# Kernel optimization log

Measured on AMD Instinct MI355X. Metric: run time of the kernel, lower is better.

Reference implementation:

```python
import jax, jax.numpy as jnp
import numpy as np

B, V, D = 8, 2048, 3
CL1_F, CL1_K = 64, 6
CL2_F, CL2_K = 128, 5
F1, F2 = 512, 256


def _uniform(k, shape, fin, fout):
    s = np.sqrt(2.0 / (fin + fout)).astype(np.float32)
    return jax.random.uniform(k, shape, jnp.float32, -s, s)


def setup_inputs() -> dict:
    key = jax.random.key(0)
    ks = jax.random.split(key, 8)
    x = jax.random.normal(ks[0], (B, D, V), jnp.float32)
    # dense stand-in for the scaled graph Laplacian; scaled so spectral radius < 1
    L = jax.random.normal(ks[1], (B, V, V), jnp.float32) * (0.5 / np.sqrt(V))
    L = 0.5 * (L + L.transpose(0, 2, 1))  # symmetric like a real Laplacian
    return {
        "x": x,
        "L": L,
        "cl1_w": _uniform(ks[2], (CL1_F, D * CL1_K), CL1_K, CL1_F),
        "cl1_b": jnp.zeros((CL1_F,), jnp.float32),
        "cl2_w": _uniform(ks[3], (CL2_F, CL2_K * CL1_F), CL2_K * CL1_F, CL2_F),
        "cl2_b": jnp.zeros((CL2_F,), jnp.float32),
        "fc1_w": _uniform(ks[4], (F1, CL2_F), CL2_F, F1),
        "fc1_b": jnp.zeros((F1,), jnp.float32),
        "fc2_w": _uniform(ks[5], (F2, F1), F1, F2),
        "fc2_b": jnp.zeros((F2,), jnp.float32),
    }


def _cheby_conv(x, L, W, b, K):
    # x: [B, V, Fin], L: [B, V, V] -> [B, V, Fout]
    x0 = x
    xs = [x0]
    if K > 1:
        x1 = jnp.einsum('bvu,buf->bvf', L, x0)
        xs.append(x1)
    for _ in range(2, K):
        x2 = 2.0 * jnp.einsum('bvu,buf->bvf', L, x1) - x0
        xs.append(x2)
        x0, x1 = x1, x2
    # torch ordering: feature index = fin * K + k  -> stack K on last axis
    xk = jnp.stack(xs, axis=-1)                 # [B, V, Fin, K]
    xk = xk.reshape(xk.shape[0], xk.shape[1], -1)  # [B, V, Fin*K]
    return xk @ W.T + b


def reference(x, L, cl1_w, cl1_b, cl2_w, cl2_b, fc1_w, fc1_b, fc2_w, fc2_b):
    xp = x.transpose(0, 2, 1)                    # [B, V, D]
    y = jax.nn.relu(_cheby_conv(xp, L, cl1_w, cl1_b, CL1_K))
    y = jax.nn.relu(_cheby_conv(y, L, cl2_w, cl2_b, CL2_K))
    y = jax.nn.relu(y @ fc1_w.T + fc1_b)
    y = jax.nn.relu(y @ fc2_w.T + fc2_b)
    return y                                     # [B, V, F2]
```

## Files before the change

kernel.cpp:

```cpp
#include <hip/hip_runtime.h>

#define B_ 8
#define V_ 2048
#define D_ 3
#define M_ (B_*V_)

typedef __attribute__((ext_vector_type(8))) short short8;
typedef __attribute__((ext_vector_type(4))) float f32x4;

__device__ inline void async_copy16(const void* g, void* lds) {
  __builtin_amdgcn_global_load_lds(
      (const __attribute__((address_space(1))) unsigned int*)g,
      (__attribute__((address_space(3))) unsigned int*)lds, 16, 0, 0);
}

__device__ inline void split_bf16(float v, short& hi, short& lo) {
  unsigned u  = __float_as_uint(v);
  unsigned hb = u & 0xFFFF0000u;
  float d = v - __uint_as_float(hb);
  hi = (short)(hb >> 16);
  lo = (short)(__float_as_uint(d) >> 16);
}

__global__ __launch_bounds__(256) void k_prep(
    const float* __restrict__ x,
    const float* __restrict__ w1, const float* __restrict__ w2,
    const float* __restrict__ fw1, const float* __restrict__ fw2,
    float* __restrict__ xa,
    short* __restrict__ XKh, short* __restrict__ XKl,
    short* __restrict__ w1h, short* __restrict__ w1l,
    short* __restrict__ w2h, short* __restrict__ w2l,
    short* __restrict__ fw1h, short* __restrict__ fw1l,
    short* __restrict__ fw2h, short* __restrict__ fw2l) {
  int i = blockIdx.x * 256 + threadIdx.x;
  short hi, lo;
  if (i < M_*64) {
    int r = i >> 6, s = i & 63;
    float val = 0.f;
    if (s == 0 || s == 6 || s == 12) {
      int f = s / 6;
      int b = r >> 11, v = r & (V_-1);
      val = x[((size_t)b*D_ + f)*V_ + v];
      xa[(size_t)r*3 + f] = val;
    }
    split_bf16(val, hi, lo);
    XKh[i] = hi; XKl[i] = lo;
    return;
  }
  i -= M_*64;
  if (i < 4096) {
    int n = i >> 6, k = i & 63;
    float v = (k < 18) ? w1[n*18 + k] : 0.f;
    split_bf16(v, hi, lo); w1h[i] = hi; w1l[i] = lo; return;
  }
  i -= 4096;
  if (i < 40960) { split_bf16(w2[i],  hi, lo); w2h[i]=hi;  w2l[i]=lo;  return; }
  i -= 40960;
  if (i < 65536) { split_bf16(fw1[i], hi, lo); fw1h[i]=hi; fw1l[i]=lo; return; }
  i -= 65536;
  if (i < 131072){ split_bf16(fw2[i], hi, lo); fw2h[i]=hi; fw2l[i]=lo; return; }
}

__global__ __launch_bounds__(256) void k_cheby1(const float* __restrict__ L,
    const float* __restrict__ xc, const float* __restrict__ xp,
    float* __restrict__ xn, short* __restrict__ XKh, short* __restrict__ XKl,
    float alpha, float beta, int kidx) {
  __shared__ float sx[3][V_];
  int b  = blockIdx.x & 7;
  int r0 = (blockIdx.x >> 3) * 16;
  const float* xcb = xc + (size_t)b*V_*D_;
  for (int i = threadIdx.x; i < V_*D_; i += 256) {
    int u = i / 3, f = i - u*3;
    sx[f][u] = xcb[i];
  }
  __syncthreads();
  int w = threadIdx.x >> 6, lane = threadIdx.x & 63;
  const float4* X0 = (const float4*)sx[0];
  const float4* X1 = (const float4*)sx[1];
  const float4* X2 = (const float4*)sx[2];
  int rbase = r0 + w*4;
  const float4* Lr[4];
  #pragma unroll
  for (int rr = 0; rr < 4; rr++)
    Lr[rr] = (const float4*)(L + ((size_t)b*V_ + rbase + rr)*V_);

  float acc[4][3] = {{0.f,0.f,0.f},{0.f,0.f,0.f},{0.f,0.f,0.f},{0.f,0.f,0.f}};

  #pragma unroll 2
  for (int it = 0; it < 8; it++) {
    int u4 = it*64 + lane;
    float4 x0 = X0[u4], x1 = X1[u4], x2 = X2[u4];
    #pragma unroll
    for (int rr = 0; rr < 4; rr++) {
      float4 lv = Lr[rr][u4];
      acc[rr][0] = fmaf(lv.x,x0.x,fmaf(lv.y,x0.y,fmaf(lv.z,x0.z,fmaf(lv.w,x0.w,acc[rr][0]))));
      acc[rr][1] = fmaf(lv.x,x1.x,fmaf(lv.y,x1.y,fmaf(lv.z,x1.z,fmaf(lv.w,x1.w,acc[rr][1]))));
      acc[rr][2] = fmaf(lv.x,x2.x,fmaf(lv.y,x2.y,fmaf(lv.z,x2.z,fmaf(lv.w,x2.w,acc[rr][2]))));
    }
  }
  #pragma unroll
  for (int off = 32; off > 0; off >>= 1)
    #pragma unroll
    for (int rr = 0; rr < 4; rr++)
      #pragma unroll
      for (int f = 0; f < 3; f++)
        acc[rr][f] += __shfl_down(acc[rr][f], off);

  if (lane == 0) {
    size_t base = ((size_t)b*V_ + rbase)*3;
    float v[12];
    #pragma unroll
    for (int rr = 0; rr < 4; rr++)
      #pragma unroll
      for (int f = 0; f < 3; f++)
        v[rr*3+f] = alpha*acc[rr][f];
    if (beta != 0.f) {
      const float4* xp4 = (const float4*)(xp + base);
      float4 p0 = xp4[0], p1 = xp4[1], p2 = xp4[2];
      v[0] -= beta*p0.x; v[1]  -= beta*p0.y; v[2]  -= beta*p0.z; v[3]  -= beta*p0.w;
      v[4] -= beta*p1.x; v[5]  -= beta*p1.y; v[6]  -= beta*p1.z; v[7]  -= beta*p1.w;
      v[8] -= beta*p2.x; v[9]  -= beta*p2.y; v[10] -= beta*p2.z; v[11] -= beta*p2.w;
    }
    float4* xn4 = (float4*)(xn + base);
    xn4[0] = make_float4(v[0], v[1], v[2],  v[3]);
    xn4[1] = make_float4(v[4], v[5], v[6],  v[7]);
    xn4[2] = make_float4(v[8], v[9], v[10], v[11]);
    #pragma unroll
    for (int rr = 0; rr < 4; rr++)
      #pragma unroll
      for (int f = 0; f < 3; f++) {
        short hi, lo; split_bf16(v[rr*3+f], hi, lo);
        size_t o = ((size_t)b*V_ + rbase + rr)*64 + f*6 + kidx;
        XKh[o] = hi; XKl[o] = lo;
      }
  }
}

__global__ __launch_bounds__(256) void k_cheby2_mfma(const float* __restrict__ L,
    const short* __restrict__ Zth, const short* __restrict__ Ztl,
    const float* __restrict__ Zp,
    float* __restrict__ Zn, short* __restrict__ ZKh, short* __restrict__ ZKl,
    short* __restrict__ Znth, short* __restrict__ Zntl,
    float alpha, float beta, int kidx) {
  __shared__ float sA[2][32*64];
  __shared__ short sBh[2][64*64];
  __shared__ short sBl[2][64*64];

  int b  = blockIdx.x & 7;
  int r0 = (blockIdx.x >> 3) * 32;
  const float* Lb   = L   + (size_t)b*V_*V_;
  const short* Zthb = Zth + (size_t)b*64*V_;
  const short* Ztlb = Ztl + (size_t)b*64*V_;

  int tid  = threadIdx.x;
  int w    = tid >> 6;
  int lane = tid & 63;
  int lm   = lane & 15;
  int quad = lane >> 4;
  int cbase = w * 16;

  int f1  = tid + 256;
  int rA0 = tid >> 4, cA0 = (tid & 15) ^ (rA0 & 15);
  int rA1 = f1 >> 4,  cA1 = (f1 & 15) ^ (rA1 & 15);
  size_t gA0 = (size_t)(r0 + rA0)*V_ + cA0*4;
  size_t gA1 = (size_t)(r0 + rA1)*V_ + cA1*4;
  int nB0 = tid >> 3, cB0 = (tid & 7) ^ (nB0 & 7);
  int nB1 = f1 >> 3,  cB1 = (f1 & 7) ^ (nB1 & 7);
  size_t gB0 = (size_t)nB0*V_ + cB0*8;
  size_t gB1 = (size_t)nB1*V_ + cB1*8;

  auto stage = [&](int bb, int k0) {
    async_copy16(Lb   + gA0 + k0, &sA[bb][tid*4]);
    async_copy16(Lb   + gA1 + k0, &sA[bb][f1*4]);
    async_copy16(Zthb + gB0 + k0, &sBh[bb][tid*8]);
    async_copy16(Ztlb + gB0 + k0, &sBl[bb][tid*8]);
    async_copy16(Zthb + gB1 + k0, &sBh[bb][f1*8]);
    async_copy16(Ztlb + gB1 + k0, &sBl[bb][f1*8]);
  };

  f32x4 acc[2] = {{0.f,0.f,0.f,0.f},{0.f,0.f,0.f,0.f}};

  stage(0, 0);

  for (int s = 0; s < V_/64; s++) {
    int bb = s & 1;
    asm volatile("s_waitcnt vmcnt(0)" ::: "memory");
    __builtin_amdgcn_s_barrier();
    __builtin_amdgcn_sched_barrier(0);
    if (s < V_/64 - 1) stage(bb ^ 1, (s+1)*64);

    const f32x4*  sAv  = (const f32x4*)sA[bb];
    const short8* sBhv = (const short8*)sBh[bb];
    const short8* sBlv = (const short8*)sBl[bb];

    #pragma unroll
    for (int ks = 0; ks < 2; ks++) {
      int koff = ks * 32;
      short8 ah[2], al[2];
      #pragma unroll
      for (int t = 0; t < 2; t++) {
        int r = t*16 + lm;
        int ca = (koff >> 2) + 2*quad;
        f32x4 a0 = sAv[r*16 + (ca ^ (r & 15))];
        f32x4 a1 = sAv[r*16 + ((ca + 1) ^ (r & 15))];
        float av[8] = {a0.x, a0.y, a0.z, a0.w, a1.x, a1.y, a1.z, a1.w};
        #pragma unroll
        for (int j = 0; j < 8; j++) {
          short hi, lo; split_bf16(av[j], hi, lo);
          ah[t][j] = hi; al[t][j] = lo;
        }
      }
      int cb = (koff >> 3) + quad;
      int n = cbase + lm;
      short8 bh = sBhv[n*8 + (cb ^ (n & 7))];
      short8 bl = sBlv[n*8 + (cb ^ (n & 7))];
      __builtin_amdgcn_s_setprio(1);
      #pragma unroll
      for (int t = 0; t < 2; t++) {
        acc[t] = __builtin_amdgcn_mfma_f32_16x16x32_bf16(ah[t], bh, acc[t], 0, 0, 0);
        acc[t] = __builtin_amdgcn_mfma_f32_16x16x32_bf16(ah[t], bl, acc[t], 0, 0, 0);
        acc[t] = __builtin_amdgcn_mfma_f32_16x16x32_bf16(al[t], bh, acc[t], 0, 0, 0);
      }
      __builtin_amdgcn_s_setprio(0);
    }
  }

  int n = cbase + lm;
  #pragma unroll
  for (int t = 0; t < 2; t++) {
    #pragma unroll
    for (int i = 0; i < 4; i++) {
      int r = r0 + t*16 + quad*4 + i;
      size_t rowb = (size_t)b*V_ + r;
      float v = alpha * acc[t][i];
      if (beta != 0.f) v -= beta * Zp[rowb*64 + n];
      Zn[rowb*64 + n] = v;
      short hi, lo; split_bf16(v, hi, lo);
      size_t ok = rowb*320 + (size_t)n*5 + kidx;
      ZKh[ok] = hi; ZKl[ok] = lo;
      size_t o = ((size_t)b*64 + n)*V_ + r;
      Znth[o] = hi; Zntl[o] = lo;
    }
  }
}

__device__ __forceinline__ void gemm_tile(
    const short* __restrict__ Ah, const short* __restrict__ Al,
    const short* __restrict__ Wh, const short* __restrict__ Wl,
    const float* __restrict__ bias, int N, int K, int row0, int col0,
    short* sAh, short* sAl, short* sWh, short* sWl,
    float* __restrict__ Cf, short* __restrict__ Ch, short* __restrict__ Cl,
    short* __restrict__ Ph, short* __restrict__ Pl, int packMul, int packStride,
    short* __restrict__ Th, short* __restrict__ Tl) {
  int tid = threadIdx.x, w = tid >> 6, lane = tid & 63;
  int lm = lane & 15, quad = lane >> 4;
  int wm = (w & 1) * 32, wn = (w >> 1) * 32;

  const short8* vAh = (const short8*)sAh;
  const short8* vAl = (const short8*)sAl;
  const short8* vWh = (const short8*)sWh;
  const short8* vWl = (const short8*)sWl;

  f32x4 acc[2][2] = {{{0.f,0.f,0.f,0.f},{0.f,0.f,0.f,0.f}},
                     {{0.f,0.f,0.f,0.f},{0.f,0.f,0.f,0.f}}};

  for (int k0 = 0; k0 < K; k0 += 64) {
    if (k0) __syncthreads();
    #pragma unroll
    for (int t = 0; t < 2; t++) {
      int f = t*256 + tid;
      int r = f >> 3, p = f & 7;
      int c = p ^ (r & 7);
      size_t goA = (size_t)(row0 + r)*K + k0 + c*8;
      size_t goW = (size_t)(col0 + r)*K + k0 + c*8;
      async_copy16(Ah + goA, &sAh[f*8]);
      async_copy16(Al + goA, &sAl[f*8]);
      async_copy16(Wh + goW, &sWh[f*8]);
      async_copy16(Wl + goW, &sWl[f*8]);
    }
    __syncthreads();

    #pragma unroll
    for (int ks = 0; ks < 2; ks++) {
      int kc = ks*4 + quad;
      short8 a_h[2], a_l[2], b_h[2], b_l[2];
      #pragma unroll
      for (int i = 0; i < 2; i++) {
        int m = wm + i*16 + lm;
        a_h[i] = vAh[m*8 + (kc ^ (m & 7))];
        a_l[i] = vAl[m*8 + (kc ^ (m & 7))];
      }
      #pragma unroll
      for (int j = 0; j < 2; j++) {
        int n = wn + j*16 + lm;
        b_h[j] = vWh[n*8 + (kc ^ (n & 7))];
        b_l[j] = vWl[n*8 + (kc ^ (n & 7))];
      }
      #pragma unroll
      for (int i = 0; i < 2; i++)
        #pragma unroll
        for (int j = 0; j < 2; j++) {
          acc[i][j] = __builtin_amdgcn_mfma_f32_16x16x32_bf16(a_h[i], b_h[j], acc[i][j], 0, 0, 0);
          acc[i][j] = __builtin_amdgcn_mfma_f32_16x16x32_bf16(a_h[i], b_l[j], acc[i][j], 0, 0, 0);
          acc[i][j] = __builtin_amdgcn_mfma_f32_16x16x32_bf16(a_l[i], b_h[j], acc[i][j], 0, 0, 0);
        }
    }
  }

  #pragma unroll
  for (int i = 0; i < 2; i++)
    #pragma unroll
    for (int j = 0; j < 2; j++) {
      int col = col0 + wn + j*16 + lm;
      float bj = bias[col];
      #pragma unroll
      for (int g = 0; g < 4; g++) {
        int row = row0 + wm + i*16 + quad*4 + g;
        float v = acc[i][j][g] + bj;
        v = v > 0.f ? v : 0.f;
        if (Cf) Cf[(size_t)row*N + col] = v;
        short hi, lo;
        if (Ch || Ph || Th) split_bf16(v, hi, lo);
        if (Ch) {
          Ch[(size_t)row*N + col] = hi;
          Cl[(size_t)row*N + col] = lo;
        }
        if (Ph) {
          size_t o = (size_t)row*packStride + (size_t)col*packMul;
          Ph[o] = hi; Pl[o] = lo;
        }
        if (Th) {
          int bb = row >> 11, vv = row & (V_-1);
          size_t o = ((size_t)bb*64 + col)*V_ + vv;
          Th[o] = hi; Tl[o] = lo;
        }
      }
    }
}

__global__ __launch_bounds__(256) void k_gemm_y1(
    const short* __restrict__ XKh, const short* __restrict__ XKl,
    const short* __restrict__ w1h, const short* __restrict__ w1l,
    const float* __restrict__ b1, float* __restrict__ y1,
    short* __restrict__ ZKh, short* __restrict__ ZKl,
    short* __restrict__ Th, short* __restrict__ Tl) {
  __shared__ short sAh[64*64], sAl[64*64], sWh[64*64], sWl[64*64];
  gemm_tile(XKh, XKl, w1h, w1l, b1, 64, 64, blockIdx.x*64, 0,
            sAh, sAl, sWh, sWl,
            y1, nullptr, nullptr, ZKh, ZKl, 5, 320, Th, Tl);
}

__global__ __launch_bounds__(256) void k_gemm_bf16(
    const short* __restrict__ Ah, const short* __restrict__ Al,
    const short* __restrict__ Wh, const short* __restrict__ Wl,
    const float* __restrict__ bias, int N, int K,
    float* __restrict__ Cf, short* __restrict__ Ch, short* __restrict__ Cl) {
  __shared__ short sAh[64*64], sAl[64*64], sWh[64*64], sWl[64*64];
  int bm = blockIdx.x & 255;
  int bn = blockIdx.x >> 8;
  gemm_tile(Ah, Al, Wh, Wl, bias, N, K, bm*64, bn*64,
            sAh, sAl, sWh, sWl,
            Cf, Ch, Cl, nullptr, nullptr, 0, 0, nullptr, nullptr);
}

extern "C" void kernel_launch(void* const* d_in, const int* in_sizes, int n_in,
                              void* d_out, int out_size, void* d_ws, size_t ws_size,
                              hipStream_t stream) {
  const float* x   = (const float*)d_in[0];
  const float* L   = (const float*)d_in[1];
  const float* w1  = (const float*)d_in[2];
  const float* b1  = (const float*)d_in[3];
  const float* w2  = (const float*)d_in[4];
  const float* b2  = (const float*)d_in[5];
  const float* fw1 = (const float*)d_in[6];
  const float* fb1 = (const float*)d_in[7];
  const float* fw2 = (const float*)d_in[8];
  const float* fb2 = (const float*)d_in[9];
  float* out = (float*)d_out;

  float* p  = (float*)d_ws;
  float* xa = p;  p += (size_t)B_*V_*D_;
  float* xb = p;  p += (size_t)B_*V_*D_;
  float* xc = p;  p += (size_t)B_*V_*D_;
  float* y1 = p;  p += (size_t)M_*64;
  float* zb = p;  p += (size_t)M_*64;
  float* zc = p;  p += (size_t)M_*64;
  short* sp = (short*)p;
  short* ZKh = sp;  sp += (size_t)M_*320;
  short* ZKl = sp;  sp += (size_t)M_*320;
  short* y2h = sp;  sp += (size_t)M_*128;
  short* y2l = sp;  sp += (size_t)M_*128;
  short* h1h = sp;  sp += (size_t)M_*512;
  short* h1l = sp;  sp += (size_t)M_*512;
  short* ZtAh = sp; sp += (size_t)M_*64;
  short* ZtAl = sp; sp += (size_t)M_*64;
  short* ZtBh = sp; sp += (size_t)M_*64;
  short* ZtBl = sp; sp += (size_t)M_*64;
  short* w1h = sp;  sp += 64*64;
  short* w1l = sp;  sp += 64*64;
  short* w2h = sp;  sp += 128*320;
  short* w2l = sp;  sp += 128*320;
  short* fw1h = sp; sp += 512*128;
  short* fw1l = sp; sp += 512*128;
  short* fw2h = sp; sp += 256*512;
  short* fw2l = sp; sp += 256*512;
  short* XKh = h1h;
  short* XKl = h1h + (size_t)M_*64;

  k_prep<<<5040, 256, 0, stream>>>(x, w1, w2, fw1, fw2, xa,
                                   XKh, XKl, w1h, w1l, w2h, w2l,
                                   fw1h, fw1l, fw2h, fw2l);

  k_cheby1<<<1024, 256, 0, stream>>>(L, xa, xa, xb, XKh, XKl, 1.f, 0.f, 1);
  k_cheby1<<<1024, 256, 0, stream>>>(L, xb, xa, xc, XKh, XKl, 2.f, 1.f, 2);
  k_cheby1<<<1024, 256, 0, stream>>>(L, xc, xb, xa, XKh, XKl, 2.f, 1.f, 3);
  k_cheby1<<<1024, 256, 0, stream>>>(L, xa, xc, xb, XKh, XKl, 2.f, 1.f, 4);
  k_cheby1<<<1024, 256, 0, stream>>>(L, xb, xa, xc, XKh, XKl, 2.f, 1.f, 5);

  k_gemm_y1<<<256, 256, 0, stream>>>(XKh, XKl, w1h, w1l, b1,
                                     y1, ZKh, ZKl, ZtAh, ZtAl);

  k_cheby2_mfma<<<512, 256, 0, stream>>>(L, ZtAh, ZtAl, y1, zb, ZKh, ZKl,
                                         ZtBh, ZtBl, 1.f, 0.f, 1);
  k_cheby2_mfma<<<512, 256, 0, stream>>>(L, ZtBh, ZtBl, y1, zc, ZKh, ZKl,
                                         ZtAh, ZtAl, 2.f, 1.f, 2);
  k_cheby2_mfma<<<512, 256, 0, stream>>>(L, ZtAh, ZtAl, zb, y1, ZKh, ZKl,
                                         ZtBh, ZtBl, 2.f, 1.f, 3);
  k_cheby2_mfma<<<512, 256, 0, stream>>>(L, ZtBh, ZtBl, zc, zb, ZKh, ZKl,
                                         ZtAh, ZtAl, 2.f, 1.f, 4);

  k_gemm_bf16<<<512, 256, 0, stream>>>(ZKh, ZKl, w2h, w2l, b2, 128, 320,
                                       nullptr, y2h, y2l);
  k_gemm_bf16<<<2048, 256, 0, stream>>>(y2h, y2l, fw1h, fw1l, fb1, 512, 128,
                                        nullptr, h1h, h1l);
  k_gemm_bf16<<<1024, 256, 0, stream>>>(h1h, h1l, fw2h, fw2l, fb2, 256, 512,
                                        out, nullptr, nullptr);
}
```

Measured before the change: 536.4 us.

## Fuse all stages into one persistent kernel with software grid barriers

Replaces the sequence of separate kernel launches with one persistent kernel of 512 blocks. The blocks step through every phase (prep, five Chebyshev-1 steps, the first GEMM, four Chebyshev-2 MFMA steps, three GEMMs) and wait at an atomic-counter grid barrier between phases. The aim is to drop per-launch overhead and the tail idle time at each kernel boundary. The cheby1 phase now processes 32 rows per block, and the GEMM phases loop over multiple tiles per block. The kernel depends on all 512 blocks being resident at once (launch_bounds 256,2) to avoid deadlock, and the shared-memory union plus fixed grid size may limit occupancy.

```diff
diff --git a/kernel.cpp b/kernel.cpp
--- a/kernel.cpp
+++ b/kernel.cpp
@@ -4,6 +4,7 @@
 #define V_ 2048
 #define D_ 3
 #define M_ (B_*V_)
+#define NBLK 512
 
 typedef __attribute__((ext_vector_type(8))) short short8;
 typedef __attribute__((ext_vector_type(4))) float f32x4;
@@ -22,77 +23,104 @@
   lo = (short)(__float_as_uint(d) >> 16);
 }
 
-__global__ __launch_bounds__(256) void k_prep(
-    const float* __restrict__ x,
-    const float* __restrict__ w1, const float* __restrict__ w2,
-    const float* __restrict__ fw1, const float* __restrict__ fw2,
-    float* __restrict__ xa,
-    short* __restrict__ XKh, short* __restrict__ XKl,
-    short* __restrict__ w1h, short* __restrict__ w1l,
-    short* __restrict__ w2h, short* __restrict__ w2l,
-    short* __restrict__ fw1h, short* __restrict__ fw1l,
-    short* __restrict__ fw2h, short* __restrict__ fw2l) {
-  int i = blockIdx.x * 256 + threadIdx.x;
-  short hi, lo;
-  if (i < M_*64) {
-    int r = i >> 6, s = i & 63;
-    float val = 0.f;
-    if (s == 0 || s == 6 || s == 12) {
-      int f = s / 6;
-      int b = r >> 11, v = r & (V_-1);
-      val = x[((size_t)b*D_ + f)*V_ + v];
-      xa[(size_t)r*3 + f] = val;
-    }
-    split_bf16(val, hi, lo);
-    XKh[i] = hi; XKl[i] = lo;
-    return;
-  }
-  i -= M_*64;
-  if (i < 4096) {
-    int n = i >> 6, k = i & 63;
-    float v = (k < 18) ? w1[n*18 + k] : 0.f;
-    split_bf16(v, hi, lo); w1h[i] = hi; w1l[i] = lo; return;
-  }
-  i -= 4096;
-  if (i < 40960) { split_bf16(w2[i],  hi, lo); w2h[i]=hi;  w2l[i]=lo;  return; }
-  i -= 40960;
-  if (i < 65536) { split_bf16(fw1[i], hi, lo); fw1h[i]=hi; fw1l[i]=lo; return; }
-  i -= 65536;
-  if (i < 131072){ split_bf16(fw2[i], hi, lo); fw2h[i]=hi; fw2l[i]=lo; return; }
-}
-
-__global__ __launch_bounds__(256) void k_cheby1(const float* __restrict__ L,
-    const float* __restrict__ xc, const float* __restrict__ xp,
-    float* __restrict__ xn, short* __restrict__ XKh, short* __restrict__ XKl,
+__device__ inline void grid_sync(unsigned* bar) {
+  __syncthreads();
+  if (threadIdx.x == 0) {
+    unsigned* cnt = bar;
+    unsigned* gen = bar + 1;
+    unsigned g = __hip_atomic_load(gen, __ATOMIC_RELAXED, __HIP_MEMORY_SCOPE_AGENT);
+    unsigned a = __hip_atomic_fetch_add(cnt, 1u, __ATOMIC_ACQ_REL, __HIP_MEMORY_SCOPE_AGENT);
+    if (a == NBLK - 1) {
+      __hip_atomic_store(cnt, 0u, __ATOMIC_RELAXED, __HIP_MEMORY_SCOPE_AGENT);
+      __hip_atomic_fetch_add(gen, 1u, __ATOMIC_ACQ_REL, __HIP_MEMORY_SCOPE_AGENT);
+    } else {
+      while (__hip_atomic_load(gen, __ATOMIC_ACQUIRE, __HIP_MEMORY_SCOPE_AGENT) == g)
+        __builtin_amdgcn_s_sleep(2);
+    }
+  }
+  __syncthreads();
+}
+
+__global__ void k_init(unsigned* bar) { bar[0] = 0u; bar[1] = 0u; }
+
+struct Params {
+  const float *x, *L, *w1, *b1, *w2, *b2, *fw1, *fb1, *fw2, *fb2;
+  float *out;
+  float *xa, *xb, *xc, *y1, *zb, *zc;
+  short *ZKh, *ZKl, *y2h, *y2l, *h1h, *h1l;
+  short *ZtAh, *ZtAl, *ZtBh, *ZtBl;
+  short *w1h, *w1l, *w2h, *w2l, *fw1h, *fw1l, *fw2h, *fw2l;
+  short *XKh, *XKl;
+  unsigned *bar;
+};
+
+union SMem {
+  float sx[3][V_];
+  struct { float a[2][32*64]; short bh[2][64*64]; short bl[2][64*64]; } c2;
+  struct { short ah[64*64]; short al[64*64]; short wh[64*64]; short wl[64*64]; } g;
+};
+
+__device__ void prep_phase(const Params& p) {
+  for (int c = 0; c < 10; c++) {
+    int i = c*131072 + blockIdx.x*256 + threadIdx.x;
+    short hi, lo;
+    if (i < M_*64) {
+      int r = i >> 6, s = i & 63;
+      float val = 0.f;
+      if (s == 0 || s == 6 || s == 12) {
+        int f = s / 6;
+        int b = r >> 11, v = r & (V_-1);
+        val = p.x[((size_t)b*D_ + f)*V_ + v];
+        p.xa[(size_t)r*3 + f] = val;
+      }
+      split_bf16(val, hi, lo);
+      p.XKh[i] = hi; p.XKl[i] = lo;
+    } else {
+      int j = i - M_*64;
+      if (j < 4096) {
+        int k = j & 63;
+        float v = (k < 18) ? p.w1[(j>>6)*18 + k] : 0.f;
+        split_bf16(v, hi, lo); p.w1h[j] = hi; p.w1l[j] = lo;
+      } else if ((j -= 4096) < 40960) {
+        split_bf16(p.w2[j],  hi, lo); p.w2h[j]=hi;  p.w2l[j]=lo;
+      } else if ((j -= 40960) < 65536) {
+        split_bf16(p.fw1[j], hi, lo); p.fw1h[j]=hi; p.fw1l[j]=lo;
+      } else if ((j -= 65536) < 131072) {
+        split_bf16(p.fw2[j], hi, lo); p.fw2h[j]=hi; p.fw2l[j]=lo;
+      }
+    }
+  }
+}
+
+__device__ void cheby1_phase(const Params& p, SMem& sm,
+    const float* xc, const float* xp, float* xn,
     float alpha, float beta, int kidx) {
-  __shared__ float sx[3][V_];
   int b  = blockIdx.x & 7;
-  int r0 = (blockIdx.x >> 3) * 16;
+  int r0 = (blockIdx.x >> 3) * 32;
   const float* xcb = xc + (size_t)b*V_*D_;
   for (int i = threadIdx.x; i < V_*D_; i += 256) {
     int u = i / 3, f = i - u*3;
-    sx[f][u] = xcb[i];
+    sm.sx[f][u] = xcb[i];
   }
   __syncthreads();
   int w = threadIdx.x >> 6, lane = threadIdx.x & 63;
-  const float4* X0 = (const float4*)sx[0];
-  const float4* X1 = (const float4*)sx[1];
-  const float4* X2 = (const float4*)sx[2];
-  int rbase = r0 + w*4;
-  const float4* Lr[4];
+  const float4* X0 = (const float4*)sm.sx[0];
+  const float4* X1 = (const float4*)sm.sx[1];
+  const float4* X2 = (const float4*)sm.sx[2];
+  int rbase = r0 + w*8;
+  const float4* Lr = (const float4*)(p.L + ((size_t)b*V_ + rbase)*V_);
+
+  float acc[8][3];
   #pragma unroll
-  for (int rr = 0; rr < 4; rr++)
-    Lr[rr] = (const float4*)(L + ((size_t)b*V_ + rbase + rr)*V_);
-
-  float acc[4][3] = {{0.f,0.f,0.f},{0.f,0.f,0.f},{0.f,0.f,0.f},{0.f,0.f,0.f}};
+  for (int rr = 0; rr < 8; rr++) { acc[rr][0]=0.f; acc[rr][1]=0.f; acc[rr][2]=0.f; }
 
   #pragma unroll 2
   for (int it = 0; it < 8; it++) {
     int u4 = it*64 + lane;
     float4 x0 = X0[u4], x1 = X1[u4], x2 = X2[u4];
     #pragma unroll
-    for (int rr = 0; rr < 4; rr++) {
-      float4 lv = Lr[rr][u4];
+    for (int rr = 0; rr < 8; rr++) {
+      float4 lv = Lr[(size_t)rr*512 + u4];
       acc[rr][0] = fmaf(lv.x,x0.x,fmaf(lv.y,x0.y,fmaf(lv.z,x0.z,fmaf(lv.w,x0.w,acc[rr][0]))));
       acc[rr][1] = fmaf(lv.x,x1.x,fmaf(lv.y,x1.y,fmaf(lv.z,x1.z,fmaf(lv.w,x1.w,acc[rr][1]))));
       acc[rr][2] = fmaf(lv.x,x2.x,fmaf(lv.y,x2.y,fmaf(lv.z,x2.z,fmaf(lv.w,x2.w,acc[rr][2]))));
@@ -101,54 +129,50 @@
   #pragma unroll
   for (int off = 32; off > 0; off >>= 1)
     #pragma unroll
-    for (int rr = 0; rr < 4; rr++)
+    for (int rr = 0; rr < 8; rr++)
       #pragma unroll
       for (int f = 0; f < 3; f++)
         acc[rr][f] += __shfl_down(acc[rr][f], off);
 
   if (lane == 0) {
     size_t base = ((size_t)b*V_ + rbase)*3;
-    float v[12];
-    #pragma unroll
-    for (int rr = 0; rr < 4; rr++)
+    float v[24];
+    #pragma unroll
+    for (int rr = 0; rr < 8; rr++)
       #pragma unroll
       for (int f = 0; f < 3; f++)
         v[rr*3+f] = alpha*acc[rr][f];
     if (beta != 0.f) {
       const float4* xp4 = (const float4*)(xp + base);
-      float4 p0 = xp4[0], p1 = xp4[1], p2 = xp4[2];
-      v[0] -= beta*p0.x; v[1]  -= beta*p0.y; v[2]  -= beta*p0.z; v[3]  -= beta*p0.w;
-      v[4] -= beta*p1.x; v[5]  -= beta*p1.y; v[6]  -= beta*p1.z; v[7]  -= beta*p1.w;
-      v[8] -= beta*p2.x; v[9]  -= beta*p2.y; v[10] -= beta*p2.z; v[11] -= beta*p2.w;
+      #pragma unroll
+      for (int q = 0; q < 6; q++) {
+        float4 pv = xp4[q];
+        v[q*4+0] -= beta*pv.x; v[q*4+1] -= beta*pv.y;
+        v[q*4+2] -= beta*pv.z; v[q*4+3] -= beta*pv.w;
+      }
     }
     float4* xn4 = (float4*)(xn + base);
-    xn4[0] = make_float4(v[0], v[1], v[2],  v[3]);
-    xn4[1] = make_float4(v[4], v[5], v[6],  v[7]);
-    xn4[2] = make_float4(v[8], v[9], v[10], v[11]);
-    #pragma unroll
-    for (int rr = 0; rr < 4; rr++)
+    #pragma unroll
+    for (int q = 0; q < 6; q++)
+      xn4[q] = make_float4(v[q*4], v[q*4+1], v[q*4+2], v[q*4+3]);
+    #pragma unroll
+    for (int rr = 0; rr < 8; rr++)
       #pragma unroll
       for (int f = 0; f < 3; f++) {
         short hi, lo; split_bf16(v[rr*3+f], hi, lo);
         size_t o = ((size_t)b*V_ + rbase + rr)*64 + f*6 + kidx;
-        XKh[o] = hi; XKl[o] = lo;
-      }
-  }
-}
-
-__global__ __launch_bounds__(256) void k_cheby2_mfma(const float* __restrict__ L,
-    const short* __restrict__ Zth, const short* __restrict__ Ztl,
-    const float* __restrict__ Zp,
-    float* __restrict__ Zn, short* __restrict__ ZKh, short* __restrict__ ZKl,
-    short* __restrict__ Znth, short* __restrict__ Zntl,
+        p.XKh[o] = hi; p.XKl[o] = lo;
+      }
+  }
+}
+
+__device__ void cheby2_phase(const Params& p, SMem& sm,
+    const short* Zth, const short* Ztl, const float* Zp,
+    float* Zn, short* Znth, short* Zntl,
     float alpha, float beta, int kidx) {
-  __shared__ float sA[2][32*64];
-  __shared__ short sBh[2][64*64];
-  __shared__ short sBl[2][64*64];
-
   int b  = blockIdx.x & 7;
   int r0 = (blockIdx.x >> 3) * 32;
-  const float* Lb   = L   + (size_t)b*V_*V_;
+  const float* Lb   = p.L + (size_t)b*V_*V_;
   const short* Zthb = Zth + (size_t)b*64*V_;
   const short* Ztlb = Ztl + (size_t)b*64*V_;
 
@@ -170,12 +194,12 @@
   size_t gB1 = (size_t)nB1*V_ + cB1*8;
 
   auto stage = [&](int bb, int k0) {
-    async_copy16(Lb   + gA0 + k0, &sA[bb][tid*4]);
-    async_copy16(Lb   + gA1 + k0, &sA[bb][f1*4]);
-    async_copy16(Zthb + gB0 + k0, &sBh[bb][tid*8]);
-    async_copy16(Ztlb + gB0 + k0, &sBl[bb][tid*8]);
-    async_copy16(Zthb + gB1 + k0, &sBh[bb][f1*8]);
-    async_copy16(Ztlb + gB1 + k0, &sBl[bb][f1*8]);
+    async_copy16(Lb   + gA0 + k0, &sm.c2.a[bb][tid*4]);
+    async_copy16(Lb   + gA1 + k0, &sm.c2.a[bb][f1*4]);
+    async_copy16(Zthb + gB0 + k0, &sm.c2.bh[bb][tid*8]);
+    async_copy16(Ztlb + gB0 + k0, &sm.c2.bl[bb][tid*8]);
+    async_copy16(Zthb + gB1 + k0, &sm.c2.bh[bb][f1*8]);
+    async_copy16(Ztlb + gB1 + k0, &sm.c2.bl[bb][f1*8]);
   };
 
   f32x4 acc[2] = {{0.f,0.f,0.f,0.f},{0.f,0.f,0.f,0.f}};
@@ -189,9 +213,9 @@
     __builtin_amdgcn_sched_barrier(0);
     if (s < V_/64 - 1) stage(bb ^ 1, (s+1)*64);
 
-    const f32x4*  sAv  = (const f32x4*)sA[bb];
-    const short8* sBhv = (const short8*)sBh[bb];
-    const short8* sBlv = (const short8*)sBl[bb];
+    const f32x4*  sAv  = (const f32x4*)sm.c2.a[bb];
+    const short8* sBhv = (const short8*)sm.c2.bh[bb];
+    const short8* sBlv = (const short8*)sm.c2.bl[bb];
 
     #pragma unroll
     for (int ks = 0; ks < 2; ks++) {
@@ -237,7 +261,7 @@
       Zn[rowb*64 + n] = v;
       short hi, lo; split_bf16(v, hi, lo);
       size_t ok = rowb*320 + (size_t)n*5 + kidx;
-      ZKh[ok] = hi; ZKl[ok] = lo;
+      p.ZKh[ok] = hi; p.ZKl[ok] = lo;
       size_t o = ((size_t)b*64 + n)*V_ + r;
       Znth[o] = hi; Zntl[o] = lo;
     }
@@ -256,6 +280,8 @@
   int lm = lane & 15, quad = lane >> 4;
   int wm = (w & 1) * 32, wn = (w >> 1) * 32;
 
+  __syncthreads();
+
   const short8* vAh = (const short8*)sAh;
   const short8* vAl = (const short8*)sAl;
   const short8* vWh = (const short8*)sWh;
@@ -269,8 +295,8 @@
     #pragma unroll
     for (int t = 0; t < 2; t++) {
       int f = t*256 + tid;
-      int r = f >> 3, p = f & 7;
-      int c = p ^ (r & 7);
+      int r = f >> 3, pp = f & 7;
+      int c = pp ^ (r & 7);
       size_t goA = (size_t)(row0 + r)*K + k0 + c*8;
       size_t goW = (size_t)(col0 + r)*K + k0 + c*8;
       async_copy16(Ah + goA, &sAh[f*8]);
@@ -338,101 +364,101 @@
     }
 }
 
-__global__ __launch_bounds__(256) void k_gemm_y1(
-    const short* __restrict__ XKh, const short* __restrict__ XKl,
-    const short* __restrict__ w1h, const short* __restrict__ w1l,
-    const float* __restrict__ b1, float* __restrict__ y1,
-    short* __restrict__ ZKh, short* __restrict__ ZKl,
-    short* __restrict__ Th, short* __restrict__ Tl) {
-  __shared__ short sAh[64*64], sAl[64*64], sWh[64*64], sWl[64*64];
-  gemm_tile(XKh, XKl, w1h, w1l, b1, 64, 64, blockIdx.x*64, 0,
-            sAh, sAl, sWh, sWl,
-            y1, nullptr, nullptr, ZKh, ZKl, 5, 320, Th, Tl);
-}
-
-__global__ __launch_bounds__(256) void k_gemm_bf16(
-    const short* __restrict__ Ah, const short* __restrict__ Al,
-    const short* __restrict__ Wh, const short* __restrict__ Wl,
-    const float* __restrict__ bias, int N, int K,
-    float* __restrict__ Cf, short* __restrict__ Ch, short* __restrict__ Cl) {
-  __shared__ short sAh[64*64], sAl[64*64], sWh[64*64], sWl[64*64];
-  int bm = blockIdx.x & 255;
-  int bn = blockIdx.x >> 8;
-  gemm_tile(Ah, Al, Wh, Wl, bias, N, K, bm*64, bn*64,
-            sAh, sAl, sWh, sWl,
-            Cf, Ch, Cl, nullptr, nullptr, 0, 0, nullptr, nullptr);
+__global__ __launch_bounds__(256, 2) void k_mega(Params p) {
+  __shared__ SMem sm;
+
+  prep_phase(p);
+  grid_sync(p.bar);
+
+  cheby1_phase(p, sm, p.xa, p.xa, p.xb, 1.f, 0.f, 1); grid_sync(p.bar);
+  cheby1_phase(p, sm, p.xb, p.xa, p.xc, 2.f, 1.f, 2); grid_sync(p.bar);
+  cheby1_phase(p, sm, p.xc, p.xb, p.xa, 2.f, 1.f, 3); grid_sync(p.bar);
+  cheby1_phase(p, sm, p.xa, p.xc, p.xb, 2.f, 1.f, 4); grid_sync(p.bar);
+  cheby1_phase(p, sm, p.xb, p.xa, p.xc, 2.f, 1.f, 5); grid_sync(p.bar);
+
+  if (blockIdx.x < 256)
+    gemm_tile(p.XKh, p.XKl, p.w1h, p.w1l, p.b1, 64, 64, blockIdx.x*64, 0,
+              sm.g.ah, sm.g.al, sm.g.wh, sm.g.wl,
+              p.y1, nullptr, nullptr, p.ZKh, p.ZKl, 5, 320, p.ZtAh, p.ZtAl);
+  grid_sync(p.bar);
+
+  cheby2_phase(p, sm, p.ZtAh, p.ZtAl, p.y1, p.zb, p.ZtBh, p.ZtBl, 1.f, 0.f, 1); grid_sync(p.bar);
+  cheby2_phase(p, sm, p.ZtBh, p.ZtBl, p.y1, p.zc, p.ZtAh, p.ZtAl, 2.f, 1.f, 2); grid_sync(p.bar);
+  cheby2_phase(p, sm, p.ZtAh, p.ZtAl, p.zb, p.y1, p.ZtBh, p.ZtBl, 2.f, 1.f, 3); grid_sync(p.bar);
+  cheby2_phase(p, sm, p.ZtBh, p.ZtBl, p.zc, p.zb, p.ZtAh, p.ZtAl, 2.f, 1.f, 4); grid_sync(p.bar);
+
+  {
+    int bm = blockIdx.x & 255, bn = blockIdx.x >> 8;
+    gemm_tile(p.ZKh, p.ZKl, p.w2h, p.w2l, p.b2, 128, 320, bm*64, bn*64,
+              sm.g.ah, sm.g.al, sm.g.wh, sm.g.wl,
+              nullptr, p.y2h, p.y2l, nullptr, nullptr, 0, 0, nullptr, nullptr);
+  }
+  grid_sync(p.bar);
+
+  for (int t = 0; t < 4; t++) {
+    int id = blockIdx.x + t*512;
+    int bm = id & 255, bn = id >> 8;
+    gemm_tile(p.y2h, p.y2l, p.fw1h, p.fw1l, p.fb1, 512, 128, bm*64, bn*64,
+              sm.g.ah, sm.g.al, sm.g.wh, sm.g.wl,
+              nullptr, p.h1h, p.h1l, nullptr, nullptr, 0, 0, nullptr, nullptr);
+  }
+  grid_sync(p.bar);
+
+  for (int t = 0; t < 2; t++) {
+    int id = blockIdx.x + t*512;
+    int bm = id & 255, bn = id >> 8;
+    gemm_tile(p.h1h, p.h1l, p.fw2h, p.fw2l, p.fb2, 256, 512, bm*64, bn*64,
+              sm.g.ah, sm.g.al, sm.g.wh, sm.g.wl,
+              p.out, nullptr, nullptr, nullptr, nullptr, 0, 0, nullptr, nullptr);
+  }
 }
 
 extern "C" void kernel_launch(void* const* d_in, const int* in_sizes, int n_in,
                               void* d_out, int out_size, void* d_ws, size_t ws_size,
                               hipStream_t stream) {
-  const float* x   = (const float*)d_in[0];
-  const float* L   = (const float*)d_in[1];
-  const float* w1  = (const float*)d_in[2];
-  const float* b1  = (const float*)d_in[3];
-  const float* w2  = (const float*)d_in[4];
-  const float* b2  = (const float*)d_in[5];
-  const float* fw1 = (const float*)d_in[6];
-  const float* fb1 = (const float*)d_in[7];
-  const float* fw2 = (const float*)d_in[8];
-  const float* fb2 = (const float*)d_in[9];
-  float* out = (float*)d_out;
+  Params pp;
+  pp.x   = (const float*)d_in[0];
+  pp.L   = (const float*)d_in[1];
+  pp.w1  = (const float*)d_in[2];
+  pp.b1  = (const float*)d_in[3];
+  pp.w2  = (const float*)d_in[4];
+  pp.b2  = (const float*)d_in[5];
+  pp.fw1 = (const float*)d_in[6];
+  pp.fb1 = (const float*)d_in[7];
+  pp.fw2 = (const float*)d_in[8];
+  pp.fb2 = (const float*)d_in[9];
+  pp.out = (float*)d_out;
 
   float* p  = (float*)d_ws;
-  float* xa = p;  p += (size_t)B_*V_*D_;
-  float* xb = p;  p += (size_t)B_*V_*D_;
-  float* xc = p;  p += (size_t)B_*V_*D_;
-  float* y1 = p;  p += (size_t)M_*64;
-  float* zb = p;  p += (size_t)M_*64;
-  float* zc = p;  p += (size_t)M_*64;
+  pp.xa = p;  p += (size_t)B_*V_*D_;
+  pp.xb = p;  p += (size_t)B_*V_*D_;
+  pp.xc = p;  p += (size_t)B_*V_*D_;
+  pp.y1 = p;  p += (size_t)M_*64;
+  pp.zb = p;  p += (size_t)M_*64;
+  pp.zc = p;  p += (size_t)M_*64;
   short* sp = (short*)p;
-  short* ZKh = sp;  sp += (size_t)M_*320;
-  short* ZKl = sp;  sp += (size_t)M_*320;
-  short* y2h = sp;  sp += (size_t)M_*128;
-  short* y2l = sp;  sp += (size_t)M_*128;
-  short* h1h = sp;  sp += (size_t)M_*512;
-  short* h1l = sp;  sp += (size_t)M_*512;
-  short* ZtAh = sp; sp += (size_t)M_*64;
-  short* ZtAl = sp; sp += (size_t)M_*64;
-  short* ZtBh = sp; sp += (size_t)M_*64;
-  short* ZtBl = sp; sp += (size_t)M_*64;
-  short* w1h = sp;  sp += 64*64;
-  short* w1l = sp;  sp += 64*64;
-  short* w2h = sp;  sp += 128*320;
-  short* w2l = sp;  sp += 128*320;
-  short* fw1h = sp; sp += 512*128;
-  short* fw1l = sp; sp += 512*128;
-  short* fw2h = sp; sp += 256*512;
-  short* fw2l = sp; sp += 256*512;
-  short* XKh = h1h;
-  short* XKl = h1h + (size_t)M_*64;
-
-  k_prep<<<5040, 256, 0, stream>>>(x, w1, w2, fw1, fw2, xa,
-                                   XKh, XKl, w1h, w1l, w2h, w2l,
-                                   fw1h, fw1l, fw2h, fw2l);
-
-  k_cheby1<<<1024, 256, 0, stream>>>(L, xa, xa, xb, XKh, XKl, 1.f, 0.f, 1);
-  k_cheby1<<<1024, 256, 0, stream>>>(L, xb, xa, xc, XKh, XKl, 2.f, 1.f, 2);
-  k_cheby1<<<1024, 256, 0, stream>>>(L, xc, xb, xa, XKh, XKl, 2.f, 1.f, 3);
-  k_cheby1<<<1024, 256, 0, stream>>>(L, xa, xc, xb, XKh, XKl, 2.f, 1.f, 4);
-  k_cheby1<<<1024, 256, 0, stream>>>(L, xb, xa, xc, XKh, XKl, 2.f, 1.f, 5);
-
-  k_gemm_y1<<<256, 256, 0, stream>>>(XKh, XKl, w1h, w1l, b1,
-                                     y1, ZKh, ZKl, ZtAh, ZtAl);
-
-  k_cheby2_mfma<<<512, 256, 0, stream>>>(L, ZtAh, ZtAl, y1, zb, ZKh, ZKl,
-                                         ZtBh, ZtBl, 1.f, 0.f, 1);
-  k_cheby2_mfma<<<512, 256, 0, stream>>>(L, ZtBh, ZtBl, y1, zc, ZKh, ZKl,
-                                         ZtAh, ZtAl, 2.f, 1.f, 2);
-  k_cheby2_mfma<<<512, 256, 0, stream>>>(L, ZtAh, ZtAl, zb, y1, ZKh, ZKl,
-                                         ZtBh, ZtBl, 2.f, 1.f, 3);
-  k_cheby2_mfma<<<512, 256, 0, stream>>>(L, ZtBh, ZtBl, zc, zb, ZKh, ZKl,
-                                         ZtAh, ZtAl, 2.f, 1.f, 4);
-
-  k_gemm_bf16<<<512, 256, 0, stream>>>(ZKh, ZKl, w2h, w2l, b2, 128, 320,
-                                       nullptr, y2h, y2l);
-  k_gemm_bf16<<<2048, 256, 0, stream>>>(y2h, y2l, fw1h, fw1l, fb1, 512, 128,
-                                        nullptr, h1h, h1l);
-  k_gemm_bf16<<<1024, 256, 0, stream>>>(h1h, h1l, fw2h, fw2l, fb2, 256, 512,
-                                        out, nullptr, nullptr);
-}
+  pp.ZKh = sp;  sp += (size_t)M_*320;
+  pp.ZKl = sp;  sp += (size_t)M_*320;
+  pp.y2h = sp;  sp += (size_t)M_*128;
+  pp.y2l = sp;  sp += (size_t)M_*128;
+  pp.h1h = sp;  sp += (size_t)M_*512;
+  pp.h1l = sp;  sp += (size_t)M_*512;
+  pp.ZtAh = sp; sp += (size_t)M_*64;
+  pp.ZtAl = sp; sp += (size_t)M_*64;
+  pp.ZtBh = sp; sp += (size_t)M_*64;
+  pp.ZtBl = sp; sp += (size_t)M_*64;
+  pp.w1h = sp;  sp += 64*64;
+  pp.w1l = sp;  sp += 64*64;
+  pp.w2h = sp;  sp += 128*320;
+  pp.w2l = sp;  sp += 128*320;
+  pp.fw1h = sp; sp += 512*128;
+  pp.fw1l = sp; sp += 512*128;
+  pp.fw2h = sp; sp += 256*512;
+  pp.fw2l = sp; sp += 256*512;
+  pp.XKh = pp.h1h;
+  pp.XKl = pp.h1h + (size_t)M_*64;
+  pp.bar = (unsigned*)((((size_t)sp) + 255) & ~(size_t)255);
+
+  k_init<<<1, 1, 0, stream>>>(pp.bar);
+  k_mega<<<NBLK, 256, 0, stream>>>(pp);
+}
```

Result: slower. 1.544 ms (+187.8%).
